# Performance work log

Hardware: AMD Instinct MI355X
Metric: run time of the kernel (lower is better)

## Reference

```python
import jax, jax.numpy as jnp
import numpy as np

N_NODES = 50000
N_EDGES = 800000
D_IN = 512
D_OUT = 128


def setup_inputs() -> dict:
    key = jax.random.key(0)
    k1, k2, k3, k4, k5 = jax.random.split(key, 5)
    x = jax.random.normal(k1, (N_NODES, D_IN), dtype=jnp.float32)
    edge_src = jax.random.randint(k2, (N_EDGES,), 0, N_NODES, dtype=jnp.int32)
    edge_dst = jnp.sort(jax.random.randint(k3, (N_EDGES,), 0, N_NODES, dtype=jnp.int32))
    edge_val = jax.random.uniform(k4, (N_EDGES,), dtype=jnp.float32)
    stdv = 1.0 / np.sqrt(D_OUT)
    weight = jax.random.uniform(k5, (D_IN, D_OUT), dtype=jnp.float32,
                                minval=-stdv, maxval=stdv)
    return {"x": x, "edge_src": edge_src, "edge_dst": edge_dst,
            "edge_val": edge_val, "weight": weight}


def reference(x, edge_src, edge_dst, edge_val, weight):
    # support = X @ W : dense GEMM [N, D_in] x [D_in, D_out]
    support = x @ weight
    # output = A @ support : SpMM via gather + weighted segment-sum over dst
    gathered = support[edge_src] * edge_val[:, None]  # [E, D_out]
    output = jax.ops.segment_sum(gathered, edge_dst, num_segments=x.shape[0])
    return output
```

## Files before the change

kernel.cpp:

```cpp
#include <hip/hip_runtime.h>
#include <hip/hip_bf16.h>

#define M_NODES 50000
#define K_DIM   512
#define N_DIM   128

typedef short s16x8 __attribute__((ext_vector_type(8)));
typedef float f32x4 __attribute__((ext_vector_type(4)));

static __device__ __forceinline__ ushort f2bf(float f) {
  uint u = __float_as_uint(f);
  u += 0x7fff + ((u >> 16) & 1);
  return (ushort)(u >> 16);
}

static __device__ __forceinline__ uint cvtpk(float lo, float hi) {
  uint r;
  asm("v_cvt_pk_bf16_f32 %0, %1, %2" : "=v"(r) : "v"(lo), "v"(hi));
  return r;
}

static __device__ __forceinline__ void g2l16(const void* g, void* l) {
  __builtin_amdgcn_global_load_lds((const __attribute__((address_space(1))) void*)g,
                                   (__attribute__((address_space(3))) void*)l, 16, 0, 0);
}

__global__ __launch_bounds__(256) void prep_zero(const float* __restrict__ W,
                                                 ushort* __restrict__ Wt,
                                                 float4* __restrict__ o4, int n4) {
  const int t = blockIdx.x * 256 + threadIdx.x;
  const int stride = gridDim.x * 256;
  for (int i = t; i < n4; i += stride) o4[i] = make_float4(0.f, 0.f, 0.f, 0.f);
  if (t < 16384) {
    int k  = t >> 5;
    int c0 = (t & 31) * 4;
    float4 v = *reinterpret_cast<const float4*>(&W[(size_t)k * N_DIM + c0]);
    Wt[(size_t)(c0 + 0) * K_DIM + k] = f2bf(v.x);
    Wt[(size_t)(c0 + 1) * K_DIM + k] = f2bf(v.y);
    Wt[(size_t)(c0 + 2) * K_DIM + k] = f2bf(v.z);
    Wt[(size_t)(c0 + 3) * K_DIM + k] = f2bf(v.w);
  }
}

#define GBK 32
#define NKS (K_DIM / GBK)

__global__ __launch_bounds__(256, 2) void gemm_mfma(const float* __restrict__ X,
                                                    const ushort* __restrict__ Wt,
                                                    float* __restrict__ S) {
  __shared__ float  Albs[2][128 * 32];
  __shared__ ushort Blbs[2][128 * 32];

  const int tid = threadIdx.x;
  const int w   = tid >> 6;
  const int l   = tid & 63;
  const int l15 = l & 15, lg = l >> 4;
  const int wr  = w >> 1, wc = w & 1;
  const int row0 = blockIdx.x * 128;

  const float* aSrc[4];
#pragma unroll
  for (int i = 0; i < 4; ++i) {
    int q = i * 256 + w * 64 + l;
    int r = q >> 3;
    int c = (q & 7) ^ (r & 7);
    int rg = row0 + r; if (rg >= M_NODES) rg = M_NODES - 1;
    aSrc[i] = X + (size_t)rg * K_DIM + c * 4;
  }
  const ushort* bSrc[2];
#pragma unroll
  for (int i = 0; i < 2; ++i) {
    int q = i * 256 + w * 64 + l;
    int col = q >> 2, j = q & 3;
    bSrc[i] = Wt + (size_t)col * K_DIM + j * 8;
  }

  f32x4 acc[4][4];
#pragma unroll
  for (int am = 0; am < 4; ++am)
#pragma unroll
    for (int bn = 0; bn < 4; ++bn) acc[am][bn] = (f32x4){0.f, 0.f, 0.f, 0.f};

#define STAGE(buf, kk) { \
  _Pragma("unroll") for (int i = 0; i < 4; ++i) \
    g2l16(aSrc[i] + (kk), (char*)&Albs[buf][0] + (size_t)(i * 256 + w * 64) * 16); \
  _Pragma("unroll") for (int i = 0; i < 2; ++i) \
    g2l16(bSrc[i] + (kk), (char*)&Blbs[buf][0] + (size_t)(i * 256 + w * 64) * 16); }

#define COMPUTE(buf) { \
  s16x8 af[4], bfr[4]; \
  _Pragma("unroll") for (int am = 0; am < 4; ++am) { \
    const int r = wr * 64 + am * 16 + l15; \
    const int s = r & 7; \
    float4 f0 = *reinterpret_cast<const float4*>(&Albs[buf][(r * 8 + ((lg * 2) ^ s)) * 4]); \
    float4 f1 = *reinterpret_cast<const float4*>(&Albs[buf][(r * 8 + ((lg * 2 + 1) ^ s)) * 4]); \
    union { s16x8 v; uint u[4]; } a; \
    a.u[0] = cvtpk(f0.x, f0.y); a.u[1] = cvtpk(f0.z, f0.w); \
    a.u[2] = cvtpk(f1.x, f1.y); a.u[3] = cvtpk(f1.z, f1.w); \
    af[am] = a.v; } \
  _Pragma("unroll") for (int bn = 0; bn < 4; ++bn) { \
    const int c = wc * 64 + bn * 16 + l15; \
    bfr[bn] = *reinterpret_cast<const s16x8*>(&Blbs[buf][c * 32 + lg * 8]); } \
  _Pragma("unroll") for (int am = 0; am < 4; ++am) \
    _Pragma("unroll") for (int bn = 0; bn < 4; ++bn) \
      acc[am][bn] = __builtin_amdgcn_mfma_f32_16x16x32_bf16(af[am], bfr[bn], acc[am][bn], 0, 0, 0); }

  STAGE(0, 0)
  __syncthreads();
#pragma unroll
  for (int t = 0; t < NKS; ++t) {
    if (t + 1 < NKS) STAGE((t + 1) & 1, (t + 1) * GBK)
    COMPUTE(t & 1)
    __syncthreads();
  }
#undef STAGE
#undef COMPUTE

#pragma unroll
  for (int am = 0; am < 4; ++am) {
#pragma unroll
    for (int rr = 0; rr < 4; ++rr) {
      const int row = row0 + wr * 64 + am * 16 + lg * 4 + rr;
      if (row < M_NODES) {
        float* sp = S + (size_t)row * N_DIM + wc * 64 + l15;
#pragma unroll
        for (int bn = 0; bn < 4; ++bn)
          sp[bn * 16] = acc[am][bn][rr];
      }
    }
  }
}

#define EPB 256
#define SBATCH 32
#define NB (EPB / SBATCH)

#define SLOAD(BUF, B) \
  _Pragma("unroll") for (int j = 0; j < SBATCH; ++j) \
    BUF[j] = S[(size_t)s_src[(B) * SBATCH + j] * N_DIM + c];

#define SPROC(BUF, B) \
  _Pragma("unroll") for (int j = 0; j < SBATCH; ++j) { \
    int d = s_dst[(B) * SBATCH + j]; \
    if (d != cur) { \
      if (cur == first) atomicAdd(&out[(size_t)cur * N_DIM + c], acc); \
      else out[(size_t)cur * N_DIM + c] = acc; \
      acc = 0.f; cur = d; \
    } \
    acc += s_val[(B) * SBATCH + j] * BUF[j]; }

__global__ __launch_bounds__(128) void spmm_edges(const float* __restrict__ S,
                                                  const int* __restrict__ esrc,
                                                  const int* __restrict__ edst,
                                                  const float* __restrict__ eval,
                                                  float* __restrict__ out) {
  __shared__ int   s_src[EPB];
  __shared__ int   s_dst[EPB];
  __shared__ float s_val[EPB];

  const int e0  = blockIdx.x * EPB;
  const int tid = threadIdx.x;

#pragma unroll
  for (int i = 0; i < EPB / 128; ++i) {
    int idx = tid + i * 128;
    s_src[idx] = esrc[e0 + idx];
    s_dst[idx] = edst[e0 + idx];
    s_val[idx] = eval[e0 + idx];
  }
  __syncthreads();

  const int c = tid;
  const int first = s_dst[0];
  float acc = 0.f;
  int   cur = first;

  float va[SBATCH], vb[SBATCH];

  SLOAD(va, 0)
#pragma unroll
  for (int b = 0; b < NB; b += 2) {
    if (b + 1 < NB) { SLOAD(vb, b + 1) }
    SPROC(va, b)
    if (b + 2 < NB) { SLOAD(va, b + 2) }
    SPROC(vb, b + 1)
  }
  atomicAdd(&out[(size_t)cur * N_DIM + c], acc);
}

extern "C" void kernel_launch(void* const* d_in, const int* in_sizes, int n_in,
                              void* d_out, int out_size, void* d_ws, size_t ws_size,
                              hipStream_t stream) {
  const float* x        = (const float*)d_in[0];
  const int*   edge_src = (const int*)d_in[1];
  const int*   edge_dst = (const int*)d_in[2];
  const float* edge_val = (const float*)d_in[3];
  const float* weight   = (const float*)d_in[4];
  float*       out      = (float*)d_out;

  float*  support = (float*)d_ws;
  ushort* wt      = (ushort*)((char*)d_ws + (size_t)M_NODES * N_DIM * 4);

  const int n_edges = in_sizes[1];

  prep_zero<<<dim3(512), dim3(256), 0, stream>>>(weight, wt, (float4*)d_out,
                                                 out_size / 4);

  gemm_mfma<<<dim3((M_NODES + 127) / 128), dim3(256), 0, stream>>>(x, wt, support);

  spmm_edges<<<dim3(n_edges / EPB), dim3(128), 0, stream>>>(support, edge_src,
                                                            edge_dst, edge_val, out);
}
```

Baseline: 241.4 us.

## Halve GEMM row tile and split SpMM edges across half-waves with float4 columns

```diff
diff --git a/kernel.cpp b/kernel.cpp
--- a/kernel.cpp
+++ b/kernel.cpp
@@ -45,10 +45,10 @@
 #define GBK 32
 #define NKS (K_DIM / GBK)
 
-__global__ __launch_bounds__(256, 2) void gemm_mfma(const float* __restrict__ X,
+__global__ __launch_bounds__(256, 4) void gemm_mfma(const float* __restrict__ X,
                                                     const ushort* __restrict__ Wt,
                                                     float* __restrict__ S) {
-  __shared__ float  Albs[2][128 * 32];
+  __shared__ float  Albs[2][64 * 32];
   __shared__ ushort Blbs[2][128 * 32];
 
   const int tid = threadIdx.x;
@@ -56,11 +56,11 @@
   const int l   = tid & 63;
   const int l15 = l & 15, lg = l >> 4;
   const int wr  = w >> 1, wc = w & 1;
-  const int row0 = blockIdx.x * 128;
-
-  const float* aSrc[4];
-#pragma unroll
-  for (int i = 0; i < 4; ++i) {
+  const int row0 = blockIdx.x * 64;
+
+  const float* aSrc[2];
+#pragma unroll
+  for (int i = 0; i < 2; ++i) {
     int q = i * 256 + w * 64 + l;
     int r = q >> 3;
     int c = (q & 7) ^ (r & 7);
@@ -75,22 +75,22 @@
     bSrc[i] = Wt + (size_t)col * K_DIM + j * 8;
   }
 
-  f32x4 acc[4][4];
-#pragma unroll
-  for (int am = 0; am < 4; ++am)
+  f32x4 acc[2][4];
+#pragma unroll
+  for (int am = 0; am < 2; ++am)
 #pragma unroll
     for (int bn = 0; bn < 4; ++bn) acc[am][bn] = (f32x4){0.f, 0.f, 0.f, 0.f};
 
 #define STAGE(buf, kk) { \
-  _Pragma("unroll") for (int i = 0; i < 4; ++i) \
+  _Pragma("unroll") for (int i = 0; i < 2; ++i) \
     g2l16(aSrc[i] + (kk), (char*)&Albs[buf][0] + (size_t)(i * 256 + w * 64) * 16); \
   _Pragma("unroll") for (int i = 0; i < 2; ++i) \
     g2l16(bSrc[i] + (kk), (char*)&Blbs[buf][0] + (size_t)(i * 256 + w * 64) * 16); }
 
 #define COMPUTE(buf) { \
-  s16x8 af[4], bfr[4]; \
-  _Pragma("unroll") for (int am = 0; am < 4; ++am) { \
-    const int r = wr * 64 + am * 16 + l15; \
+  s16x8 af[2], bfr[4]; \
+  _Pragma("unroll") for (int am = 0; am < 2; ++am) { \
+    const int r = wr * 32 + am * 16 + l15; \
     const int s = r & 7; \
     float4 f0 = *reinterpret_cast<const float4*>(&Albs[buf][(r * 8 + ((lg * 2) ^ s)) * 4]); \
     float4 f1 = *reinterpret_cast<const float4*>(&Albs[buf][(r * 8 + ((lg * 2 + 1) ^ s)) * 4]); \
@@ -101,7 +101,7 @@
   _Pragma("unroll") for (int bn = 0; bn < 4; ++bn) { \
     const int c = wc * 64 + bn * 16 + l15; \
     bfr[bn] = *reinterpret_cast<const s16x8*>(&Blbs[buf][c * 32 + lg * 8]); } \
-  _Pragma("unroll") for (int am = 0; am < 4; ++am) \
+  _Pragma("unroll") for (int am = 0; am < 2; ++am) \
     _Pragma("unroll") for (int bn = 0; bn < 4; ++bn) \
       acc[am][bn] = __builtin_amdgcn_mfma_f32_16x16x32_bf16(af[am], bfr[bn], acc[am][bn], 0, 0, 0); }
 
@@ -117,10 +117,10 @@
 #undef COMPUTE
 
 #pragma unroll
-  for (int am = 0; am < 4; ++am) {
+  for (int am = 0; am < 2; ++am) {
 #pragma unroll
     for (int rr = 0; rr < 4; ++rr) {
-      const int row = row0 + wr * 64 + am * 16 + lg * 4 + rr;
+      const int row = row0 + wr * 32 + am * 16 + lg * 4 + rr;
       if (row < M_NODES) {
         float* sp = S + (size_t)row * N_DIM + wc * 64 + l15;
 #pragma unroll
@@ -132,28 +132,14 @@
 }
 
 #define EPB 256
-#define SBATCH 32
-#define NB (EPB / SBATCH)
-
-#define SLOAD(BUF, B) \
-  _Pragma("unroll") for (int j = 0; j < SBATCH; ++j) \
-    BUF[j] = S[(size_t)s_src[(B) * SBATCH + j] * N_DIM + c];
-
-#define SPROC(BUF, B) \
-  _Pragma("unroll") for (int j = 0; j < SBATCH; ++j) { \
-    int d = s_dst[(B) * SBATCH + j]; \
-    if (d != cur) { \
-      if (cur == first) atomicAdd(&out[(size_t)cur * N_DIM + c], acc); \
-      else out[(size_t)cur * N_DIM + c] = acc; \
-      acc = 0.f; cur = d; \
-    } \
-    acc += s_val[(B) * SBATCH + j] * BUF[j]; }
-
-__global__ __launch_bounds__(128) void spmm_edges(const float* __restrict__ S,
-                                                  const int* __restrict__ esrc,
-                                                  const int* __restrict__ edst,
-                                                  const float* __restrict__ eval,
-                                                  float* __restrict__ out) {
+#define CHUNK 64
+#define SB 8
+
+__global__ __launch_bounds__(128, 4) void spmm_edges(const float* __restrict__ S,
+                                                     const int* __restrict__ esrc,
+                                                     const int* __restrict__ edst,
+                                                     const float* __restrict__ eval,
+                                                     float* __restrict__ out) {
   __shared__ int   s_src[EPB];
   __shared__ int   s_dst[EPB];
   __shared__ float s_val[EPB];
@@ -170,22 +156,60 @@
   }
   __syncthreads();
 
-  const int c = tid;
-  const int first = s_dst[0];
-  float acc = 0.f;
+  const int wid  = tid >> 6;
+  const int l    = tid & 63;
+  const int half = (wid << 1) | (l >> 5);
+  const int hl   = l & 31;
+  const int base = half * CHUNK;
+  const int c0   = hl * 4;
+
+  const int first = s_dst[base];
   int   cur = first;
-
-  float va[SBATCH], vb[SBATCH];
-
-  SLOAD(va, 0)
-#pragma unroll
-  for (int b = 0; b < NB; b += 2) {
-    if (b + 1 < NB) { SLOAD(vb, b + 1) }
-    SPROC(va, b)
-    if (b + 2 < NB) { SLOAD(va, b + 2) }
-    SPROC(vb, b + 1)
-  }
-  atomicAdd(&out[(size_t)cur * N_DIM + c], acc);
+  f32x4 acc = {0.f, 0.f, 0.f, 0.f};
+
+  f32x4 bufA[SB], bufB[SB];
+
+#define SLOAD(BUF, B) { \
+  _Pragma("unroll") for (int j = 0; j < SB; ++j) \
+    BUF[j] = *reinterpret_cast<const f32x4*>( \
+        S + (size_t)s_src[base + (B) * SB + j] * N_DIM + c0); \
+  __builtin_amdgcn_sched_barrier(0); }
+
+#define FLUSH() { \
+  float* op = out + (size_t)cur * N_DIM + c0; \
+  if (cur == first) { \
+    atomicAdd(op + 0, acc[0]); atomicAdd(op + 1, acc[1]); \
+    atomicAdd(op + 2, acc[2]); atomicAdd(op + 3, acc[3]); \
+  } else { \
+    *reinterpret_cast<f32x4*>(op) = acc; \
+  } \
+  acc = (f32x4){0.f, 0.f, 0.f, 0.f}; }
+
+#define SPROC(BUF, B) { \
+  _Pragma("unroll") for (int j = 0; j < SB; ++j) { \
+    const int e = base + (B) * SB + j; \
+    const int d = s_dst[e]; \
+    if (d != cur) { FLUSH() cur = d; } \
+    const float vv = s_val[e]; \
+    acc[0] += vv * BUF[j][0]; acc[1] += vv * BUF[j][1]; \
+    acc[2] += vv * BUF[j][2]; acc[3] += vv * BUF[j][3]; } }
+
+  SLOAD(bufA, 0)
+#pragma unroll
+  for (int b = 0; b < CHUNK / SB; b += 2) {
+    if (b + 1 < CHUNK / SB) SLOAD(bufB, b + 1)
+    SPROC(bufA, b)
+    if (b + 2 < CHUNK / SB) SLOAD(bufA, b + 2)
+    SPROC(bufB, b + 1)
+  }
+  {
+    float* op = out + (size_t)cur * N_DIM + c0;
+    atomicAdd(op + 0, acc[0]); atomicAdd(op + 1, acc[1]);
+    atomicAdd(op + 2, acc[2]); atomicAdd(op + 3, acc[3]);
+  }
+#undef SLOAD
+#undef SPROC
+#undef FLUSH
 }
 
 extern "C" void kernel_launch(void* const* d_in, const int* in_sizes, int n_in,
@@ -206,7 +230,7 @@
   prep_zero<<<dim3(512), dim3(256), 0, stream>>>(weight, wt, (float4*)d_out,
                                                  out_size / 4);
 
-  gemm_mfma<<<dim3((M_NODES + 127) / 128), dim3(256), 0, stream>>>(x, wt, support);
+  gemm_mfma<<<dim3((M_NODES + 63) / 64), dim3(256), 0, stream>>>(x, wt, support);
 
   spmm_edges<<<dim3(n_edges / EPB), dim3(128), 0, stream>>>(support, edge_src,
                                                             edge_dst, edge_val, out);
```

Measured after the change: 251.0 us. +4.0%, slower.
